# Optimization experiments

Measured on AMD Instinct MI355X. Metric: run time of the kernel, lower is better.

## Reference

```python
import jax, jax.numpy as jnp
import numpy as np

B = 1024
INPUT_DIM = 768
NUM_CLASSES = 5
NUM_PRIMARY_CAPS = 32
PRIMARY_CAP_DIM = 8
ROUTING_CAP_DIM = 16
NUM_ITER = 3
PROJ_DIM = 256 * 6 * 6  # 9216
NUM_IN_CAPS = NUM_PRIMARY_CAPS * 16  # conv output is 4x4 spatial -> 512


def squash(t, axis=-1):
    sq = jnp.sum(t * t, axis=axis, keepdims=True)
    scale = sq / (1.0 + sq)
    return scale * t / jnp.sqrt(sq + 1e-8)


def setup_inputs() -> dict:
    key = jax.random.key(0)
    k = jax.random.split(key, 6)
    x = jax.random.normal(k[0], (B, INPUT_DIM), dtype=jnp.float32)
    W1 = jax.random.normal(k[1], (INPUT_DIM, PROJ_DIM), dtype=jnp.float32) * 0.02
    b1 = jnp.zeros((PROJ_DIM,), dtype=jnp.float32)
    convW = jax.random.normal(k[2], (NUM_PRIMARY_CAPS * PRIMARY_CAP_DIM, 256, 3, 3), dtype=jnp.float32) * 0.02  # OIHW
    convB = jnp.zeros((NUM_PRIMARY_CAPS * PRIMARY_CAP_DIM,), dtype=jnp.float32)
    # matches torch.randn init in RoutingCapsules: [num_in, num_out, out_dim, in_dim]
    Wr = jax.random.normal(k[3], (NUM_IN_CAPS, NUM_CLASSES, ROUTING_CAP_DIM, PRIMARY_CAP_DIM), dtype=jnp.float32)
    return {"x": x, "W1": W1, "b1": b1, "convW": convW, "convB": convB, "Wr": Wr}


def reference(x, W1, b1, convW, convB, Wr):
    # feature projection (dropout is identity in eval)
    h = jax.nn.relu(x @ W1 + b1)
    h = h.reshape(-1, 256, 6, 6)
    # primary capsules conv: k=3, s=1, pad=0 -> [B, 256, 4, 4]
    out = jax.lax.conv_general_dilated(h, convW, window_strides=(1, 1), padding='VALID',
                                       dimension_numbers=('NCHW', 'OIHW', 'NCHW'))
    out = out + convB[None, :, None, None]
    bsz = out.shape[0]
    out = out.reshape(bsz, NUM_PRIMARY_CAPS, PRIMARY_CAP_DIM, -1)      # [B,32,8,16]
    out = jnp.transpose(out, (0, 1, 3, 2)).reshape(bsz, -1, PRIMARY_CAP_DIM)  # [B,512,8]
    u = squash(out, axis=-1)
    # prediction vectors u_hat: [B, in_caps, out_caps, out_dim]
    u_hat = jnp.einsum('nodi,bni->bnod', Wr, u)
    # dynamic routing
    b_logits = jnp.zeros((bsz, NUM_IN_CAPS, NUM_CLASSES, 1), dtype=u_hat.dtype)
    v = None
    for it in range(NUM_ITER):
        c = jax.nn.softmax(b_logits, axis=2)
        s = jnp.sum(c * u_hat, axis=1)  # [B, out_caps, out_dim]
        v = squash(s, axis=-1)
        if it < NUM_ITER - 1:
            agreement = jnp.sum(u_hat * v[:, None], axis=-1, keepdims=True)
            b_logits = b_logits + agreement
    class_probs = jnp.sqrt(jnp.sum(v * v, axis=-1))
    return (class_probs, v)
```

## Files before the change

kernel.cpp:

```cpp
#include <hip/hip_runtime.h>
#include <hip/hip_fp16.h>

#define BSZ   1024
#define INDIM 768
#define PROJ  9216
#define NCAP  512
#define NCLS  5
#define K2    2304

typedef __bf16    bf16x8 __attribute__((ext_vector_type(8)));
typedef _Float16  f16x8  __attribute__((ext_vector_type(8)));
typedef float     f32x4  __attribute__((ext_vector_type(4)));
typedef _Float16  h2     __attribute__((ext_vector_type(2)));

static __device__ __forceinline__ unsigned short f2bf(float f) {
  unsigned int x = __float_as_uint(f);
  return (unsigned short)((x + 0x7fffu + ((x >> 16) & 1u)) >> 16);
}
static __device__ __forceinline__ float bf2f(unsigned int u) {
  return __uint_as_float(u << 16);
}

#if defined(__has_builtin)
#if __has_builtin(__builtin_amdgcn_fdot2)
#define HAVE_FDOT2 1
#endif
#endif
static __device__ __forceinline__ float fdot2(h2 a, h2 b, float c) {
#ifdef HAVE_FDOT2
  return __builtin_amdgcn_fdot2(a, b, c, false);
#else
  return c + (float)a[0] * (float)b[0] + (float)a[1] * (float)b[1];
#endif
}
static __device__ __forceinline__ h2 u2h2(unsigned int u) {
  return __builtin_bit_cast(h2, u);
}
static __device__ __forceinline__ unsigned short f2h(float f) {
  return __builtin_bit_cast(unsigned short, (_Float16)f);
}

static __device__ __forceinline__ void gload16(const void* g, void* l) {
  auto gp = reinterpret_cast<const unsigned int __attribute__((address_space(1)))*>(
      (unsigned long long)g);
  auto lp = reinterpret_cast<unsigned int __attribute__((address_space(3)))*>(
      (unsigned long long)l);
  __builtin_amdgcn_global_load_lds(gp, lp, 16, 0, 0);
}

template <int RELU, int OBF16>
__global__ __launch_bounds__(256) void mfma_gemm(
    const unsigned short* __restrict__ A,
    const unsigned short* __restrict__ Bt,
    const float* __restrict__ bias,
    void* __restrict__ Cout,
    int M, int N, int K) {
  __shared__ __align__(16) unsigned short smem[16384];
  const int t    = threadIdx.x;
  const int bn   = blockIdx.x * 128;
  const int bm   = blockIdx.y * 128;
  const int lane = t & 63;
  const int wid  = t >> 6;
  const int wm   = (wid >> 1) * 64;
  const int wn   = (wid & 1) * 64;
  const int l15  = lane & 15;
  const int kb   = lane >> 4;

  const int r0 = t >> 2,         kc = t & 3;
  const int r1 = (t + 256) >> 2;
  const int gk0 = ((kc ^ (r0 & 3)) << 3);
  const int gk1 = ((kc ^ (r1 & 3)) << 3);

  const unsigned short* Ar0 = A  + (size_t)(bm + r0) * K + gk0;
  const unsigned short* Ar1 = A  + (size_t)(bm + r1) * K + gk1;
  const unsigned short* Br0 = Bt + (size_t)(bn + r0) * K + gk0;
  const unsigned short* Br1 = Bt + (size_t)(bn + r1) * K + gk1;

  int aoff[4], boff[4];
#pragma unroll
  for (int i = 0; i < 4; ++i) {
    const int ra = wm + i * 16 + l15;
    aoff[i] = ra * 32 + ((kb ^ (ra & 3)) << 3);
    const int rb = wn + i * 16 + l15;
    boff[i] = 4096 + rb * 32 + ((kb ^ (rb & 3)) << 3);
  }

  f32x4 acc[4][4];
#pragma unroll
  for (int i = 0; i < 4; ++i)
#pragma unroll
    for (int j = 0; j < 4; ++j)
#pragma unroll
      for (int q = 0; q < 4; ++q) acc[i][j][q] = 0.f;

  const int nk = K >> 5;
  gload16(Ar0, &smem[t * 8]);
  gload16(Ar1, &smem[(t + 256) * 8]);
  gload16(Br0, &smem[4096 + t * 8]);
  gload16(Br1, &smem[4096 + (t + 256) * 8]);
  __syncthreads();

  int buf = 0;
  for (int ks = 0; ks < nk; ++ks) {
    if (ks + 1 < nk) {
      const int k = (ks + 1) << 5;
      const int o = (buf ^ 1) * 8192;
      gload16(Ar0 + k, &smem[o + t * 8]);
      gload16(Ar1 + k, &smem[o + (t + 256) * 8]);
      gload16(Br0 + k, &smem[o + 4096 + t * 8]);
      gload16(Br1 + k, &smem[o + 4096 + (t + 256) * 8]);
    }
    const unsigned short* base = &smem[buf * 8192];
    bf16x8 af[4], bfr[4];
#pragma unroll
    for (int i = 0; i < 4; ++i) {
      af[i]  = *(const bf16x8*)(base + aoff[i]);
      bfr[i] = *(const bf16x8*)(base + boff[i]);
    }
#pragma unroll
    for (int i = 0; i < 4; ++i)
#pragma unroll
      for (int j = 0; j < 4; ++j)
        acc[i][j] = __builtin_amdgcn_mfma_f32_16x16x32_bf16(af[i], bfr[j], acc[i][j], 0, 0, 0);
    __syncthreads();
    buf ^= 1;
  }

#pragma unroll
  for (int j = 0; j < 4; ++j) {
    const int col = bn + wn + j * 16 + l15;
    const float bv = bias[col];
#pragma unroll
    for (int i = 0; i < 4; ++i) {
#pragma unroll
      for (int q = 0; q < 4; ++q) {
        const int row = bm + wm + i * 16 + kb * 4 + q;
        float v = acc[i][j][q] + bv;
        if (RELU) v = fmaxf(v, 0.f);
        if (OBF16) ((unsigned short*)Cout)[(size_t)row * N + col] = f2bf(v);
        else       ((float*)Cout)[(size_t)row * N + col] = v;
      }
    }
  }
}

__global__ __launch_bounds__(256) void conv_gemm_sq(
    const unsigned short* __restrict__ ht,
    const unsigned short* __restrict__ Wt2,
    const float* __restrict__ convB,
    unsigned short* __restrict__ U) {
  __shared__ __align__(16) unsigned short smem[24576];
  const int t    = threadIdx.x;
  const int bn   = blockIdx.x * 128;
  const int bm   = blockIdx.y * 64;
  const int lane = t & 63, wid = t >> 6;
  const int l15  = lane & 15, kb = lane >> 4;

  const unsigned short* asrc[2];
#pragma unroll
  for (int cc = 0; cc < 2; ++cc) {
    const int c = t + cc * 256;
    const int row = c >> 3, seg = c & 7;
    const int gr = bm + row, b = gr >> 4, p = gr & 15;
    const int spb = (p >> 2) * 6 + (p & 3);
    asrc[cc] = ht + (size_t)b * PROJ + spb * 256 + ((seg ^ (row & 7)) << 3);
  }
  const unsigned short* bsrc[4];
#pragma unroll
  for (int cc = 0; cc < 4; ++cc) {
    const int c = t + cc * 256;
    const int row = c >> 3, seg = c & 7;
    bsrc[cc] = Wt2 + (size_t)(bn + row) * K2 + ((seg ^ (row & 7)) << 3);
  }

  int aoff[4][2], boff[2][2];
#pragma unroll
  for (int i = 0; i < 4; ++i)
#pragma unroll
    for (int kk = 0; kk < 2; ++kk) {
      const int row = i * 16 + l15, seg = kk * 4 + kb;
      aoff[i][kk] = row * 64 + ((seg ^ (row & 7)) << 3);
    }
#pragma unroll
  for (int j = 0; j < 2; ++j)
#pragma unroll
    for (int kk = 0; kk < 2; ++kk) {
      const int row = wid * 32 + j * 16 + l15, seg = kk * 4 + kb;
      boff[j][kk] = 4096 + row * 64 + ((seg ^ (row & 7)) << 3);
    }

  f32x4 acc[4][2];
#pragma unroll
  for (int i = 0; i < 4; ++i)
#pragma unroll
    for (int j = 0; j < 2; ++j)
#pragma unroll
      for (int q = 0; q < 4; ++q) acc[i][j][q] = 0.f;

  auto stage = [&](int ks, int buf) {
    const int tap  = ks >> 2;
    const int aofs = (tap + 3 * (tap / 3)) * 256 + ((ks & 3) << 6);
    const int bofs = ks << 6;
    unsigned short* sb = &smem[buf * 12288];
    gload16(asrc[0] + aofs, sb + t * 8);
    gload16(asrc[1] + aofs, sb + t * 8 + 2048);
    gload16(bsrc[0] + bofs, sb + 4096 + t * 8);
    gload16(bsrc[1] + bofs, sb + 4096 + t * 8 + 2048);
    gload16(bsrc[2] + bofs, sb + 4096 + t * 8 + 4096);
    gload16(bsrc[3] + bofs, sb + 4096 + t * 8 + 6144);
  };

  stage(0, 0);
  __syncthreads();

  int buf = 0;
  for (int ks = 0; ks < 36; ++ks) {
    if (ks + 1 < 36) stage(ks + 1, buf ^ 1);
    const unsigned short* base = &smem[buf * 12288];
    bf16x8 af[4][2], bfr[2][2];
#pragma unroll
    for (int i = 0; i < 4; ++i)
#pragma unroll
      for (int kk = 0; kk < 2; ++kk) af[i][kk] = *(const bf16x8*)(base + aoff[i][kk]);
#pragma unroll
    for (int j = 0; j < 2; ++j)
#pragma unroll
      for (int kk = 0; kk < 2; ++kk) bfr[j][kk] = *(const bf16x8*)(base + boff[j][kk]);
#pragma unroll
    for (int kk = 0; kk < 2; ++kk)
#pragma unroll
      for (int i = 0; i < 4; ++i)
#pragma unroll
        for (int j = 0; j < 2; ++j)
          acc[i][j] = __builtin_amdgcn_mfma_f32_16x16x32_bf16(af[i][kk], bfr[j][kk], acc[i][j], 0, 0, 0);
    __syncthreads();
    buf ^= 1;
  }

#pragma unroll
  for (int j = 0; j < 2; ++j) {
    const int oc  = bn + wid * 32 + j * 16 + l15;
    const int cap = oc >> 3, ii = oc & 7;
    const float bv = convB[oc];
#pragma unroll
    for (int i = 0; i < 4; ++i) {
#pragma unroll
      for (int q = 0; q < 4; ++q) {
        const int row = bm + i * 16 + kb * 4 + q;
        const int b = row >> 4, p = row & 15;
        const float val = acc[i][j][q] + bv;
        float sq = val * val;
        sq += __shfl_xor(sq, 1);
        sq += __shfl_xor(sq, 2);
        sq += __shfl_xor(sq, 4);
        const float scale = sq / (1.f + sq) / sqrtf(sq + 1e-8f);
        U[(size_t)b * 4096 + cap * 128 + p * 8 + ii] = f2h(val * scale);
      }
    }
  }
}

__global__ __launch_bounds__(256) void convert_bf16(const float* __restrict__ in,
                                                    unsigned short* __restrict__ out,
                                                    int n4) {
  const int i = blockIdx.x * 256 + threadIdx.x;
  if (i >= n4) return;
  float4 v = ((const float4*)in)[i];
  ushort4 o;
  o.x = f2bf(v.x); o.y = f2bf(v.y); o.z = f2bf(v.z); o.w = f2bf(v.w);
  ((ushort4*)out)[i] = o;
}

__global__ __launch_bounds__(256) void convert_f16(const float* __restrict__ in,
                                                   __half2* __restrict__ out, int n4) {
  const int i = blockIdx.x * 256 + threadIdx.x;
  if (i >= n4) return;
  float4 v = ((const float4*)in)[i];
  out[i * 2]     = __floats2half2_rn(v.x, v.y);
  out[i * 2 + 1] = __floats2half2_rn(v.z, v.w);
}

__global__ __launch_bounds__(256) void transpose_w1_perm(const float* __restrict__ W,
                                                         unsigned short* __restrict__ Wt) {
  __shared__ float tile[32][33];
  const int n0 = blockIdx.x * 32, k0 = blockIdx.y * 32;
  const int r = threadIdx.x >> 3, c = (threadIdx.x & 7) * 4;
  float4 v = *(const float4*)(W + (size_t)(k0 + r) * PROJ + n0 + c);
  tile[r][c] = v.x; tile[r][c + 1] = v.y; tile[r][c + 2] = v.z; tile[r][c + 3] = v.w;
  __syncthreads();
  ushort4 o;
  o.x = f2bf(tile[c + 0][r]); o.y = f2bf(tile[c + 1][r]);
  o.z = f2bf(tile[c + 2][r]); o.w = f2bf(tile[c + 3][r]);
  const int nn = n0 + r;
  const int prow = (nn % 36) * 256 + nn / 36;
  *(ushort4*)(Wt + (size_t)prow * INDIM + k0 + c) = o;
}

__global__ __launch_bounds__(256) void perm_bias(const float* __restrict__ b1,
                                                 float* __restrict__ pb1) {
  const int n = blockIdx.x * 256 + threadIdx.x;
  if (n >= PROJ) return;
  pb1[(n % 36) * 256 + n / 36] = b1[n];
}

__global__ __launch_bounds__(256) void convw_prep2(const float* __restrict__ W,
                                                   unsigned short* __restrict__ Wt2) {
  const int id = blockIdx.x * 256 + threadIdx.x;
  const int oc = id >> 8, ic = id & 255;
  const float* s = W + (size_t)id * 9;
#pragma unroll
  for (int tap = 0; tap < 9; ++tap)
    Wt2[(size_t)oc * K2 + tap * 256 + ic] = f2bf(s[tap]);
}

__global__ __launch_bounds__(512) void uhat_gemm(
    const unsigned short* __restrict__ U,
    const unsigned short* __restrict__ Wrh,
    unsigned short* __restrict__ uhat,
    float* __restrict__ s0q,
    int b0, int CB) {
  __shared__ float sred[8][16][80];
  const int mt = blockIdx.x, q = blockIdx.y;
  const int t = threadIdx.x, wid = t >> 6, lane = t & 63;
  const int l15 = lane & 15, kb = lane >> 4;
  const int bm = mt * 16;
  const int gb = b0 + bm;

  f32x4 sacc[5];
#pragma unroll
  for (int j = 0; j < 5; ++j)
#pragma unroll
    for (int r = 0; r < 4; ++r) sacc[j][r] = 0.f;

  const uint4 zz = make_uint4(0, 0, 0, 0);
#pragma unroll
  for (int i = 0; i < 8; ++i) {
    const int n = q * 64 + wid * 8 + i;
    uint4 av = zz;
    if (kb == 0) av = *(const uint4*)(U + (size_t)(gb + l15) * 4096 + n * 8);
    const f16x8 uf = __builtin_bit_cast(f16x8, av);
#pragma unroll
    for (int jn = 0; jn < 5; ++jn) {
      uint4 wv = zz;
      if (kb == 0) wv = *(const uint4*)(Wrh + (size_t)n * 640 + (jn * 16 + l15) * 8);
      f32x4 z;
      z[0] = 0.f; z[1] = 0.f; z[2] = 0.f; z[3] = 0.f;
      f32x4 c = __builtin_amdgcn_mfma_f32_16x16x32_f16(
          __builtin_bit_cast(f16x8, wv), uf, z, 0, 0, 0);
      ushort4 st;
      st.x = f2h(c[0]); st.y = f2h(c[1]); st.z = f2h(c[2]); st.w = f2h(c[3]);
      *(ushort4*)(uhat + ((size_t)(bm + l15) * 512 + n) * 80 + jn * 16 + kb * 4) = st;
#pragma unroll
      for (int qq = 0; qq < 4; ++qq) sacc[jn][qq] += c[qq];
    }
  }

#pragma unroll
  for (int jn = 0; jn < 5; ++jn)
#pragma unroll
    for (int qq = 0; qq < 4; ++qq)
      sred[wid][l15][jn * 16 + kb * 4 + qq] = sacc[jn][qq];
  __syncthreads();
#pragma unroll
  for (int k = 0; k < 3; ++k) {
    const int id = t + k * 512;
    if (id < 1280) {
      const int bb = id / 80, od = id % 80;
      float val = 0.f;
#pragma unroll
      for (int w = 0; w < 8; ++w) val += sred[w][bb][od];
      s0q[((size_t)q * CB + bm + bb) * 80 + od] = val;
    }
  }
}

template <int MODE>
__global__ __launch_bounds__(256) void route_pass(
    const unsigned short* __restrict__ uhat,
    const float* __restrict__ s0q,
    const float* __restrict__ vsum_in,
    float* __restrict__ vsum_out,
    float* __restrict__ out,
    int b0, int CB) {
  __shared__ unsigned int vph2[40];
  __shared__ float red[4][2][40];
  const int bl = blockIdx.x;
  const int b  = b0 + bl;
  const int t  = threadIdx.x;

  float v0r = 0.f;
  if (t < 80) {
    if (MODE == 1) {
      float s = 0.f;
#pragma unroll
      for (int g = 0; g < 8; ++g) s += s0q[((size_t)g * CB + bl) * 80 + t];
      s *= 0.2f;
      float sq = s * s;
      sq += __shfl_xor(sq, 1);
      sq += __shfl_xor(sq, 2);
      sq += __shfl_xor(sq, 4);
      sq += __shfl_xor(sq, 8);
      const float scale = sq / (1.f + sq) / sqrtf(sq + 1e-8f);
      v0r = s * scale;
    } else {
      v0r = vsum_in[(size_t)bl * 80 + t];
    }
    const float vnext = __shfl_down(v0r, 1);
    if ((t & 1) == 0)
      vph2[t >> 1] = __builtin_bit_cast(unsigned int, __floats2half2_rn(v0r, vnext));
  }
  __syncthreads();

  const int p = t >> 1, h = t & 1;
  float acc[5][8];
#pragma unroll
  for (int o = 0; o < 5; ++o)
#pragma unroll
    for (int j = 0; j < 8; ++j) acc[o][j] = 0.f;

  const unsigned short* ub = uhat + (size_t)bl * 40960;
  for (int c4 = 0; c4 < 4; ++c4) {
    const int n = c4 * 128 + p;
    const unsigned short* row = ub + n * 80 + h * 8;
    uint4 uv[5];
#pragma unroll
    for (int o = 0; o < 5; ++o) uv[o] = *(const uint4*)(row + o * 16);
    float ap[5];
#pragma unroll
    for (int o = 0; o < 5; ++o) {
      const int vb = o * 8 + h * 4;
      float a = fdot2(u2h2(uv[o].x), u2h2(vph2[vb]), 0.f);
      a = fdot2(u2h2(uv[o].y), u2h2(vph2[vb + 1]), a);
      a = fdot2(u2h2(uv[o].z), u2h2(vph2[vb + 2]), a);
      a = fdot2(u2h2(uv[o].w), u2h2(vph2[vb + 3]), a);
      ap[o] = a + __shfl_xor(a, 1);
    }
    float m = ap[0];
#pragma unroll
    for (int o = 1; o < 5; ++o) m = fmaxf(m, ap[o]);
    float es = 0.f, e[5];
#pragma unroll
    for (int o = 0; o < 5; ++o) { e[o] = __expf(ap[o] - m); es += e[o]; }
    const float inv = 1.f / es;
#pragma unroll
    for (int o = 0; o < 5; ++o) {
      const float cc = e[o] * inv;
      h2 hx = u2h2(uv[o].x), hy = u2h2(uv[o].y), hz = u2h2(uv[o].z), hw = u2h2(uv[o].w);
      acc[o][0] += cc * (float)hx[0]; acc[o][1] += cc * (float)hx[1];
      acc[o][2] += cc * (float)hy[0]; acc[o][3] += cc * (float)hy[1];
      acc[o][4] += cc * (float)hz[0]; acc[o][5] += cc * (float)hz[1];
      acc[o][6] += cc * (float)hw[0]; acc[o][7] += cc * (float)hw[1];
    }
  }

#pragma unroll
  for (int off = 2; off <= 32; off <<= 1)
#pragma unroll
    for (int o = 0; o < 5; ++o)
#pragma unroll
      for (int j = 0; j < 8; ++j) acc[o][j] += __shfl_xor(acc[o][j], off);
  const int wid = t >> 6, lane = t & 63;
  if (lane < 2) {
#pragma unroll
    for (int o = 0; o < 5; ++o)
#pragma unroll
      for (int j = 0; j < 8; ++j) red[wid][lane][o * 8 + j] = acc[o][j];
  }
  __syncthreads();

  if (t < 80) {
    const int o = t >> 4, d = t & 15, hh = d >> 3, dl = d & 7;
    const int c = o * 8 + dl;
    float s = red[0][hh][c] + red[1][hh][c] + red[2][hh][c] + red[3][hh][c];
    float sq = s * s;
    sq += __shfl_xor(sq, 1);
    sq += __shfl_xor(sq, 2);
    sq += __shfl_xor(sq, 4);
    sq += __shfl_xor(sq, 8);
    const float scale = sq / (1.f + sq) / sqrtf(sq + 1e-8f);
    const float vn = s * scale;
    if (MODE == 1) {
      vsum_out[(size_t)bl * 80 + t] = v0r + vn;
    } else {
      out[5 * BSZ + (size_t)b * 80 + t] = vn;
      float vv = vn * vn;
      vv += __shfl_xor(vv, 1);
      vv += __shfl_xor(vv, 2);
      vv += __shfl_xor(vv, 4);
      vv += __shfl_xor(vv, 8);
      if ((t & 15) == 0) out[(size_t)b * 5 + o] = sqrtf(vv);
    }
  }
}

extern "C" void kernel_launch(void* const* d_in, const int* in_sizes, int n_in,
                              void* d_out, int out_size, void* d_ws, size_t ws_size,
                              hipStream_t stream) {
  const float* x     = (const float*)d_in[0];
  const float* W1    = (const float*)d_in[1];
  const float* b1    = (const float*)d_in[2];
  const float* convW = (const float*)d_in[3];
  const float* convB = (const float*)d_in[4];
  const float* Wr    = (const float*)d_in[5];
  float* out = (float*)d_out;

  char* base = (char*)d_ws;
  size_t off = 0;
  auto alloc = [&](size_t bytes) { size_t o = off; off = (off + bytes + 255) & ~(size_t)255; return o; };
  const size_t o_wrh  = alloc((size_t)NCAP * 640 * 2);
  const size_t o_u    = alloc((size_t)BSZ * 4096 * 2);
  const size_t o_s0q  = alloc((size_t)8 * BSZ * 80 * 4);
  const size_t o_vsum = alloc((size_t)BSZ * 80 * 4);
  const size_t o_pool = off;
  size_t poff = o_pool;
  auto palloc = [&](size_t bytes) { size_t o = poff; poff = (poff + bytes + 255) & ~(size_t)255; return o; };
  const size_t o_ht  = palloc((size_t)BSZ * PROJ * 2);
  const size_t o_w1t = palloc((size_t)PROJ * INDIM * 2);
  const size_t o_xb  = palloc((size_t)BSZ * INDIM * 2);
  const size_t o_wt2 = palloc((size_t)256 * K2 * 2);
  const size_t o_pb1 = palloc((size_t)PROJ * 4);

  unsigned short* ht   = (unsigned short*)(base + o_ht);
  unsigned short* w1t  = (unsigned short*)(base + o_w1t);
  unsigned short* xb   = (unsigned short*)(base + o_xb);
  unsigned short* wt2  = (unsigned short*)(base + o_wt2);
  float*          pb1  = (float*)(base + o_pb1);
  unsigned short* wrh  = (unsigned short*)(base + o_wrh);
  unsigned short* u    = (unsigned short*)(base + o_u);
  float*          s0q  = (float*)(base + o_s0q);
  float*          vsum = (float*)(base + o_vsum);
  unsigned short* uhat = (unsigned short*)(base + o_pool);

  convert_bf16<<<(BSZ * INDIM / 4 + 255) / 256, 256, 0, stream>>>(x, xb, BSZ * INDIM / 4);
  transpose_w1_perm<<<dim3(PROJ / 32, INDIM / 32), 256, 0, stream>>>(W1, w1t);
  perm_bias<<<PROJ / 256, 256, 0, stream>>>(b1, pb1);
  convw_prep2<<<256, 256, 0, stream>>>(convW, wt2);
  convert_f16<<<(NCAP * 640 / 4 + 255) / 256, 256, 0, stream>>>(Wr, (__half2*)wrh, NCAP * 640 / 4);

  mfma_gemm<1, 1><<<dim3(PROJ / 128, BSZ / 128), 256, 0, stream>>>(
      xb, w1t, pb1, (void*)ht, BSZ, PROJ, INDIM);

  conv_gemm_sq<<<dim3(2, 256), 256, 0, stream>>>(ht, wt2, convB, u);

  const size_t pool_sz = ws_size > o_pool ? ws_size - o_pool : 0;
  int CB = 1024;
  while (CB > 16 && (size_t)CB * 512 * 80 * 2 > pool_sz) CB >>= 1;
  for (int b0 = 0; b0 < BSZ; b0 += CB) {
    uhat_gemm<<<dim3(CB / 16, 8), 512, 0, stream>>>(
        u, wrh, uhat, s0q, b0, CB);
    route_pass<1><<<CB, 256, 0, stream>>>(uhat, s0q, nullptr, vsum, out, b0, CB);
    route_pass<2><<<CB, 256, 0, stream>>>(uhat, nullptr, vsum, nullptr, out, b0, CB);
  }
}
```

Baseline: 152.8 us.

## Recompute u_hat per routing pass instead of materializing it in memory

Replaces the stored fp16 u_hat tensor with on-the-fly MFMA recomputation inside three fused routing kernels. Each pass rebuilds the previous v from per-group partial sums, computes agreement and softmax in registers, and writes new partial sums. This removes the large u_hat write and two rereads in exchange for redundant small GEMMs. The small preprocessing kernels are also merged into a single launch.

Result: slower. 157.0 us (+2.7%).

```diff
diff --git a/kernel.cpp b/kernel.cpp
--- a/kernel.cpp
+++ b/kernel.cpp
@@ -19,22 +19,6 @@
 }
 static __device__ __forceinline__ float bf2f(unsigned int u) {
   return __uint_as_float(u << 16);
-}
-
-#if defined(__has_builtin)
-#if __has_builtin(__builtin_amdgcn_fdot2)
-#define HAVE_FDOT2 1
-#endif
-#endif
-static __device__ __forceinline__ float fdot2(h2 a, h2 b, float c) {
-#ifdef HAVE_FDOT2
-  return __builtin_amdgcn_fdot2(a, b, c, false);
-#else
-  return c + (float)a[0] * (float)b[0] + (float)a[1] * (float)b[1];
-#endif
-}
-static __device__ __forceinline__ h2 u2h2(unsigned int u) {
-  return __builtin_bit_cast(h2, u);
 }
 static __device__ __forceinline__ unsigned short f2h(float f) {
   return __builtin_bit_cast(unsigned short, (_Float16)f);
@@ -260,24 +244,39 @@
   }
 }
 
-__global__ __launch_bounds__(256) void convert_bf16(const float* __restrict__ in,
-                                                    unsigned short* __restrict__ out,
-                                                    int n4) {
-  const int i = blockIdx.x * 256 + threadIdx.x;
-  if (i >= n4) return;
-  float4 v = ((const float4*)in)[i];
-  ushort4 o;
-  o.x = f2bf(v.x); o.y = f2bf(v.y); o.z = f2bf(v.z); o.w = f2bf(v.w);
-  ((ushort4*)out)[i] = o;
-}
-
-__global__ __launch_bounds__(256) void convert_f16(const float* __restrict__ in,
-                                                   __half2* __restrict__ out, int n4) {
-  const int i = blockIdx.x * 256 + threadIdx.x;
-  if (i >= n4) return;
-  float4 v = ((const float4*)in)[i];
-  out[i * 2]     = __floats2half2_rn(v.x, v.y);
-  out[i * 2 + 1] = __floats2half2_rn(v.z, v.w);
+#define NX_ITEMS (BSZ * INDIM / 4)
+#define NW_ITEMS (NCAP * 640 / 4)
+#define NC_ITEMS 65536
+#define NB_ITEMS PROJ
+#define PREP_TOTAL (NX_ITEMS + NW_ITEMS + NC_ITEMS + NB_ITEMS)
+
+__global__ __launch_bounds__(256) void prep_small(
+    const float* __restrict__ x, unsigned short* __restrict__ xb,
+    const float* __restrict__ Wr, __half2* __restrict__ wrh,
+    const float* __restrict__ convW, unsigned short* __restrict__ wt2,
+    const float* __restrict__ b1, float* __restrict__ pb1) {
+  const int id = blockIdx.x * 256 + threadIdx.x;
+  if (id < NX_ITEMS) {
+    float4 v = ((const float4*)x)[id];
+    ushort4 o;
+    o.x = f2bf(v.x); o.y = f2bf(v.y); o.z = f2bf(v.z); o.w = f2bf(v.w);
+    ((ushort4*)xb)[id] = o;
+  } else if (id < NX_ITEMS + NW_ITEMS) {
+    const int i = id - NX_ITEMS;
+    float4 v = ((const float4*)Wr)[i];
+    wrh[i * 2]     = __floats2half2_rn(v.x, v.y);
+    wrh[i * 2 + 1] = __floats2half2_rn(v.z, v.w);
+  } else if (id < NX_ITEMS + NW_ITEMS + NC_ITEMS) {
+    const int i = id - NX_ITEMS - NW_ITEMS;
+    const int oc = i >> 8, ic = i & 255;
+    const float* s = convW + (size_t)i * 9;
+#pragma unroll
+    for (int tap = 0; tap < 9; ++tap)
+      wt2[(size_t)oc * K2 + tap * 256 + ic] = f2bf(s[tap]);
+  } else if (id < PREP_TOTAL) {
+    const int n = id - NX_ITEMS - NW_ITEMS - NC_ITEMS;
+    pb1[(n % 36) * 256 + n / 36] = b1[n];
+  }
 }
 
 __global__ __launch_bounds__(256) void transpose_w1_perm(const float* __restrict__ W,
@@ -296,41 +295,68 @@
   *(ushort4*)(Wt + (size_t)prow * INDIM + k0 + c) = o;
 }
 
-__global__ __launch_bounds__(256) void perm_bias(const float* __restrict__ b1,
-                                                 float* __restrict__ pb1) {
-  const int n = blockIdx.x * 256 + threadIdx.x;
-  if (n >= PROJ) return;
-  pb1[(n % 36) * 256 + n / 36] = b1[n];
-}
-
-__global__ __launch_bounds__(256) void convw_prep2(const float* __restrict__ W,
-                                                   unsigned short* __restrict__ Wt2) {
-  const int id = blockIdx.x * 256 + threadIdx.x;
-  const int oc = id >> 8, ic = id & 255;
-  const float* s = W + (size_t)id * 9;
-#pragma unroll
-  for (int tap = 0; tap < 9; ++tap)
-    Wt2[(size_t)oc * K2 + tap * 256 + ic] = f2bf(s[tap]);
-}
-
-__global__ __launch_bounds__(512) void uhat_gemm(
+template <int MODE>
+__global__ __launch_bounds__(512) void route_fused(
     const unsigned short* __restrict__ U,
     const unsigned short* __restrict__ Wrh,
-    unsigned short* __restrict__ uhat,
-    float* __restrict__ s0q,
-    int b0, int CB) {
+    const float* __restrict__ sp0,
+    const float* __restrict__ sp1,
+    float* __restrict__ spout) {
   __shared__ float sred[8][16][80];
+  __shared__ float s0l[16][81];
+  __shared__ float s1l[16][81];
+  __shared__ float scl[16][5][2];
   const int mt = blockIdx.x, q = blockIdx.y;
   const int t = threadIdx.x, wid = t >> 6, lane = t & 63;
   const int l15 = lane & 15, kb = lane >> 4;
-  const int bm = mt * 16;
-  const int gb = b0 + bm;
+  const int gb = mt * 16;
+
+  float vreg[5][4];
+  if (MODE >= 1) {
+    for (int item = t; item < 1280; item += 512) {
+      const int bl = item / 80, od = item % 80;
+      float a0 = 0.f, a1 = 0.f;
+#pragma unroll
+      for (int g = 0; g < 8; ++g) {
+        a0 += sp0[((size_t)g * BSZ + gb + bl) * 80 + od];
+        if (MODE == 2) a1 += sp1[((size_t)g * BSZ + gb + bl) * 80 + od];
+      }
+      s0l[bl][od] = a0 * 0.2f;
+      if (MODE == 2) s1l[bl][od] = a1;
+    }
+    __syncthreads();
+    if (t < 80) {
+      const int bl = t / 5, o = t % 5;
+      float sq0 = 0.f, sq1 = 0.f;
+#pragma unroll
+      for (int d = 0; d < 16; ++d) {
+        const float x0 = s0l[bl][o * 16 + d];
+        sq0 += x0 * x0;
+        if (MODE == 2) { const float x1 = s1l[bl][o * 16 + d]; sq1 += x1 * x1; }
+      }
+      scl[bl][o][0] = sq0 / (1.f + sq0) / sqrtf(sq0 + 1e-8f);
+      if (MODE == 2) scl[bl][o][1] = sq1 / (1.f + sq1) / sqrtf(sq1 + 1e-8f);
+    }
+    __syncthreads();
+#pragma unroll
+    for (int jn = 0; jn < 5; ++jn) {
+      const float sc0 = scl[l15][jn][0];
+      const float sc1 = (MODE == 2) ? scl[l15][jn][1] : 0.f;
+#pragma unroll
+      for (int qq = 0; qq < 4; ++qq) {
+        const int od = jn * 16 + kb * 4 + qq;
+        float v = s0l[l15][od] * sc0;
+        if (MODE == 2) v += s1l[l15][od] * sc1;
+        vreg[jn][qq] = v;
+      }
+    }
+  }
 
   f32x4 sacc[5];
 #pragma unroll
-  for (int j = 0; j < 5; ++j)
-#pragma unroll
-    for (int r = 0; r < 4; ++r) sacc[j][r] = 0.f;
+  for (int jn = 0; jn < 5; ++jn)
+#pragma unroll
+    for (int qq = 0; qq < 4; ++qq) sacc[jn][qq] = 0.f;
 
   const uint4 zz = make_uint4(0, 0, 0, 0);
 #pragma unroll
@@ -339,20 +365,42 @@
     uint4 av = zz;
     if (kb == 0) av = *(const uint4*)(U + (size_t)(gb + l15) * 4096 + n * 8);
     const f16x8 uf = __builtin_bit_cast(f16x8, av);
+    f32x4 cfr[5];
 #pragma unroll
     for (int jn = 0; jn < 5; ++jn) {
       uint4 wv = zz;
       if (kb == 0) wv = *(const uint4*)(Wrh + (size_t)n * 640 + (jn * 16 + l15) * 8);
       f32x4 z;
       z[0] = 0.f; z[1] = 0.f; z[2] = 0.f; z[3] = 0.f;
-      f32x4 c = __builtin_amdgcn_mfma_f32_16x16x32_f16(
+      cfr[jn] = __builtin_amdgcn_mfma_f32_16x16x32_f16(
           __builtin_bit_cast(f16x8, wv), uf, z, 0, 0, 0);
-      ushort4 st;
-      st.x = f2h(c[0]); st.y = f2h(c[1]); st.z = f2h(c[2]); st.w = f2h(c[3]);
-      *(ushort4*)(uhat + ((size_t)(bm + l15) * 512 + n) * 80 + jn * 16 + kb * 4) = st;
-#pragma unroll
-      for (int qq = 0; qq < 4; ++qq) sacc[jn][qq] += c[qq];
-    }
+    }
+    float c[5];
+    if (MODE == 0) {
+#pragma unroll
+      for (int o = 0; o < 5; ++o) c[o] = 1.f;
+    } else {
+      float a[5];
+#pragma unroll
+      for (int jn = 0; jn < 5; ++jn) {
+        float d = cfr[jn][0] * vreg[jn][0] + cfr[jn][1] * vreg[jn][1] +
+                  cfr[jn][2] * vreg[jn][2] + cfr[jn][3] * vreg[jn][3];
+        d += __shfl_xor(d, 16);
+        d += __shfl_xor(d, 32);
+        a[jn] = d;
+      }
+      float m = fmaxf(fmaxf(fmaxf(a[0], a[1]), fmaxf(a[2], a[3])), a[4]);
+      float es = 0.f;
+#pragma unroll
+      for (int o = 0; o < 5; ++o) { c[o] = __expf(a[o] - m); es += c[o]; }
+      const float inv = 1.f / es;
+#pragma unroll
+      for (int o = 0; o < 5; ++o) c[o] *= inv;
+    }
+#pragma unroll
+    for (int jn = 0; jn < 5; ++jn)
+#pragma unroll
+      for (int qq = 0; qq < 4; ++qq) sacc[jn][qq] += c[jn] * cfr[jn][qq];
   }
 
 #pragma unroll
@@ -369,109 +417,18 @@
       float val = 0.f;
 #pragma unroll
       for (int w = 0; w < 8; ++w) val += sred[w][bb][od];
-      s0q[((size_t)q * CB + bm + bb) * 80 + od] = val;
-    }
-  }
-}
-
-template <int MODE>
-__global__ __launch_bounds__(256) void route_pass(
-    const unsigned short* __restrict__ uhat,
-    const float* __restrict__ s0q,
-    const float* __restrict__ vsum_in,
-    float* __restrict__ vsum_out,
-    float* __restrict__ out,
-    int b0, int CB) {
-  __shared__ unsigned int vph2[40];
-  __shared__ float red[4][2][40];
-  const int bl = blockIdx.x;
-  const int b  = b0 + bl;
-  const int t  = threadIdx.x;
-
-  float v0r = 0.f;
+      spout[((size_t)q * BSZ + gb + bb) * 80 + od] = val;
+    }
+  }
+}
+
+__global__ __launch_bounds__(128) void route_emit(
+    const float* __restrict__ sp2, float* __restrict__ out) {
+  const int b = blockIdx.x, t = threadIdx.x;
   if (t < 80) {
-    if (MODE == 1) {
-      float s = 0.f;
-#pragma unroll
-      for (int g = 0; g < 8; ++g) s += s0q[((size_t)g * CB + bl) * 80 + t];
-      s *= 0.2f;
-      float sq = s * s;
-      sq += __shfl_xor(sq, 1);
-      sq += __shfl_xor(sq, 2);
-      sq += __shfl_xor(sq, 4);
-      sq += __shfl_xor(sq, 8);
-      const float scale = sq / (1.f + sq) / sqrtf(sq + 1e-8f);
-      v0r = s * scale;
-    } else {
-      v0r = vsum_in[(size_t)bl * 80 + t];
-    }
-    const float vnext = __shfl_down(v0r, 1);
-    if ((t & 1) == 0)
-      vph2[t >> 1] = __builtin_bit_cast(unsigned int, __floats2half2_rn(v0r, vnext));
-  }
-  __syncthreads();
-
-  const int p = t >> 1, h = t & 1;
-  float acc[5][8];
-#pragma unroll
-  for (int o = 0; o < 5; ++o)
-#pragma unroll
-    for (int j = 0; j < 8; ++j) acc[o][j] = 0.f;
-
-  const unsigned short* ub = uhat + (size_t)bl * 40960;
-  for (int c4 = 0; c4 < 4; ++c4) {
-    const int n = c4 * 128 + p;
-    const unsigned short* row = ub + n * 80 + h * 8;
-    uint4 uv[5];
-#pragma unroll
-    for (int o = 0; o < 5; ++o) uv[o] = *(const uint4*)(row + o * 16);
-    float ap[5];
-#pragma unroll
-    for (int o = 0; o < 5; ++o) {
-      const int vb = o * 8 + h * 4;
-      float a = fdot2(u2h2(uv[o].x), u2h2(vph2[vb]), 0.f);
-      a = fdot2(u2h2(uv[o].y), u2h2(vph2[vb + 1]), a);
-      a = fdot2(u2h2(uv[o].z), u2h2(vph2[vb + 2]), a);
-      a = fdot2(u2h2(uv[o].w), u2h2(vph2[vb + 3]), a);
-      ap[o] = a + __shfl_xor(a, 1);
-    }
-    float m = ap[0];
-#pragma unroll
-    for (int o = 1; o < 5; ++o) m = fmaxf(m, ap[o]);
-    float es = 0.f, e[5];
-#pragma unroll
-    for (int o = 0; o < 5; ++o) { e[o] = __expf(ap[o] - m); es += e[o]; }
-    const float inv = 1.f / es;
-#pragma unroll
-    for (int o = 0; o < 5; ++o) {
-      const float cc = e[o] * inv;
-      h2 hx = u2h2(uv[o].x), hy = u2h2(uv[o].y), hz = u2h2(uv[o].z), hw = u2h2(uv[o].w);
-      acc[o][0] += cc * (float)hx[0]; acc[o][1] += cc * (float)hx[1];
-      acc[o][2] += cc * (float)hy[0]; acc[o][3] += cc * (float)hy[1];
-      acc[o][4] += cc * (float)hz[0]; acc[o][5] += cc * (float)hz[1];
-      acc[o][6] += cc * (float)hw[0]; acc[o][7] += cc * (float)hw[1];
-    }
-  }
-
-#pragma unroll
-  for (int off = 2; off <= 32; off <<= 1)
-#pragma unroll
-    for (int o = 0; o < 5; ++o)
-#pragma unroll
-      for (int j = 0; j < 8; ++j) acc[o][j] += __shfl_xor(acc[o][j], off);
-  const int wid = t >> 6, lane = t & 63;
-  if (lane < 2) {
-#pragma unroll
-    for (int o = 0; o < 5; ++o)
-#pragma unroll
-      for (int j = 0; j < 8; ++j) red[wid][lane][o * 8 + j] = acc[o][j];
-  }
-  __syncthreads();
-
-  if (t < 80) {
-    const int o = t >> 4, d = t & 15, hh = d >> 3, dl = d & 7;
-    const int c = o * 8 + dl;
-    float s = red[0][hh][c] + red[1][hh][c] + red[2][hh][c] + red[3][hh][c];
+    float s = 0.f;
+#pragma unroll
+    for (int g = 0; g < 8; ++g) s += sp2[((size_t)g * BSZ + b) * 80 + t];
     float sq = s * s;
     sq += __shfl_xor(sq, 1);
     sq += __shfl_xor(sq, 2);
@@ -479,17 +436,13 @@
     sq += __shfl_xor(sq, 8);
     const float scale = sq / (1.f + sq) / sqrtf(sq + 1e-8f);
     const float vn = s * scale;
-    if (MODE == 1) {
-      vsum_out[(size_t)bl * 80 + t] = v0r + vn;
-    } else {
-      out[5 * BSZ + (size_t)b * 80 + t] = vn;
-      float vv = vn * vn;
-      vv += __shfl_xor(vv, 1);
-      vv += __shfl_xor(vv, 2);
-      vv += __shfl_xor(vv, 4);
-      vv += __shfl_xor(vv, 8);
-      if ((t & 15) == 0) out[(size_t)b * 5 + o] = sqrtf(vv);
-    }
+    out[5 * BSZ + (size_t)b * 80 + t] = vn;
+    float vv = vn * vn;
+    vv += __shfl_xor(vv, 1);
+    vv += __shfl_xor(vv, 2);
+    vv += __shfl_xor(vv, 4);
+    vv += __shfl_xor(vv, 8);
+    if ((t & 15) == 0) out[(size_t)b * 5 + (t >> 4)] = sqrtf(vv);
   }
 }
 
@@ -507,48 +460,40 @@
   char* base = (char*)d_ws;
   size_t off = 0;
   auto alloc = [&](size_t bytes) { size_t o = off; off = (off + bytes + 255) & ~(size_t)255; return o; };
-  const size_t o_wrh  = alloc((size_t)NCAP * 640 * 2);
-  const size_t o_u    = alloc((size_t)BSZ * 4096 * 2);
-  const size_t o_s0q  = alloc((size_t)8 * BSZ * 80 * 4);
-  const size_t o_vsum = alloc((size_t)BSZ * 80 * 4);
-  const size_t o_pool = off;
-  size_t poff = o_pool;
-  auto palloc = [&](size_t bytes) { size_t o = poff; poff = (poff + bytes + 255) & ~(size_t)255; return o; };
-  const size_t o_ht  = palloc((size_t)BSZ * PROJ * 2);
-  const size_t o_w1t = palloc((size_t)PROJ * INDIM * 2);
-  const size_t o_xb  = palloc((size_t)BSZ * INDIM * 2);
-  const size_t o_wt2 = palloc((size_t)256 * K2 * 2);
-  const size_t o_pb1 = palloc((size_t)PROJ * 4);
-
-  unsigned short* ht   = (unsigned short*)(base + o_ht);
-  unsigned short* w1t  = (unsigned short*)(base + o_w1t);
-  unsigned short* xb   = (unsigned short*)(base + o_xb);
-  unsigned short* wt2  = (unsigned short*)(base + o_wt2);
-  float*          pb1  = (float*)(base + o_pb1);
-  unsigned short* wrh  = (unsigned short*)(base + o_wrh);
-  unsigned short* u    = (unsigned short*)(base + o_u);
-  float*          s0q  = (float*)(base + o_s0q);
-  float*          vsum = (float*)(base + o_vsum);
-  unsigned short* uhat = (unsigned short*)(base + o_pool);
-
-  convert_bf16<<<(BSZ * INDIM / 4 + 255) / 256, 256, 0, stream>>>(x, xb, BSZ * INDIM / 4);
+  const size_t o_wrh = alloc((size_t)NCAP * 640 * 2);
+  const size_t o_u   = alloc((size_t)BSZ * 4096 * 2);
+  const size_t o_sp0 = alloc((size_t)8 * BSZ * 80 * 4);
+  const size_t o_sp1 = alloc((size_t)8 * BSZ * 80 * 4);
+  const size_t o_sp2 = alloc((size_t)8 * BSZ * 80 * 4);
+  const size_t o_ht  = alloc((size_t)BSZ * PROJ * 2);
+  const size_t o_w1t = alloc((size_t)PROJ * INDIM * 2);
+  const size_t o_xb  = alloc((size_t)BSZ * INDIM * 2);
+  const size_t o_wt2 = alloc((size_t)256 * K2 * 2);
+  const size_t o_pb1 = alloc((size_t)PROJ * 4);
+
+  unsigned short* wrh = (unsigned short*)(base + o_wrh);
+  unsigned short* u   = (unsigned short*)(base + o_u);
+  float*          sp0 = (float*)(base + o_sp0);
+  float*          sp1 = (float*)(base + o_sp1);
+  float*          sp2 = (float*)(base + o_sp2);
+  unsigned short* ht  = (unsigned short*)(base + o_ht);
+  unsigned short* w1t = (unsigned short*)(base + o_w1t);
+  unsigned short* xb  = (unsigned short*)(base + o_xb);
+  unsigned short* wt2 = (unsigned short*)(base + o_wt2);
+  float*          pb1 = (float*)(base + o_pb1);
+
+  prep_small<<<(PREP_TOTAL + 255) / 256, 256, 0, stream>>>(
+      x, xb, Wr, (__half2*)wrh, convW, wt2, b1, pb1);
   transpose_w1_perm<<<dim3(PROJ / 32, INDIM / 32), 256, 0, stream>>>(W1, w1t);
-  perm_bias<<<PROJ / 256, 256, 0, stream>>>(b1, pb1);
-  convw_prep2<<<256, 256, 0, stream>>>(convW, wt2);
-  convert_f16<<<(NCAP * 640 / 4 + 255) / 256, 256, 0, stream>>>(Wr, (__half2*)wrh, NCAP * 640 / 4);
 
   mfma_gemm<1, 1><<<dim3(PROJ / 128, BSZ / 128), 256, 0, stream>>>(
       xb, w1t, pb1, (void*)ht, BSZ, PROJ, INDIM);
 
   conv_gemm_sq<<<dim3(2, 256), 256, 0, stream>>>(ht, wt2, convB, u);
 
-  const size_t pool_sz = ws_size > o_pool ? ws_size - o_pool : 0;
-  int CB = 1024;
-  while (CB > 16 && (size_t)CB * 512 * 80 * 2 > pool_sz) CB >>= 1;
-  for (int b0 = 0; b0 < BSZ; b0 += CB) {
-    uhat_gemm<<<dim3(CB / 16, 8), 512, 0, stream>>>(
-        u, wrh, uhat, s0q, b0, CB);
-    route_pass<1><<<CB, 256, 0, stream>>>(uhat, s0q, nullptr, vsum, out, b0, CB);
-    route_pass<2><<<CB, 256, 0, stream>>>(uhat, nullptr, vsum, nullptr, out, b0, CB);
-  }
-}
+  dim3 fg(BSZ / 16, 8);
+  route_fused<0><<<fg, 512, 0, stream>>>(u, wrh, nullptr, nullptr, sp0);
+  route_fused<1><<<fg, 512, 0, stream>>>(u, wrh, sp0, nullptr, sp1);
+  route_fused<2><<<fg, 512, 0, stream>>>(u, wrh, sp0, sp1, sp2);
+  route_emit<<<BSZ, 128, 0, stream>>>(sp2, out);
+}
```

## Deepen GEMM K-tile to 64, enlarge conv tile to 128x128, fuse prep kernels

Applied to the files above, without the earlier changes.

The projection GEMM now stages 64-wide K slices with an XOR swizzle over 8 segments, which halves the number of loop iterations and barriers. The conv GEMM moves from a 64x128 to a 128x128 block tile with a 2x2 wave layout, giving more reuse per LDS load. Four small preprocessing kernels are merged into one launch to cut launch overhead. In exchange, each block uses more LDS (64KB) and more accumulator registers, which may lower occupancy, and the conv grid is halved.

Result: slower. 157.0 us (+2.8%).

```diff
diff --git a/kernel.cpp b/kernel.cpp
--- a/kernel.cpp
+++ b/kernel.cpp
@@ -19,6 +19,9 @@
 }
 static __device__ __forceinline__ float bf2f(unsigned int u) {
   return __uint_as_float(u << 16);
+}
+static __device__ __forceinline__ unsigned short f2h(float f) {
+  return __builtin_bit_cast(unsigned short, (_Float16)f);
 }
 
 #if defined(__has_builtin)
@@ -36,9 +39,6 @@
 static __device__ __forceinline__ h2 u2h2(unsigned int u) {
   return __builtin_bit_cast(h2, u);
 }
-static __device__ __forceinline__ unsigned short f2h(float f) {
-  return __builtin_bit_cast(unsigned short, (_Float16)f);
-}
 
 static __device__ __forceinline__ void gload16(const void* g, void* l) {
   auto gp = reinterpret_cast<const unsigned int __attribute__((address_space(1)))*>(
@@ -48,42 +48,42 @@
   __builtin_amdgcn_global_load_lds(gp, lp, 16, 0, 0);
 }
 
-template <int RELU, int OBF16>
-__global__ __launch_bounds__(256) void mfma_gemm(
+__global__ __launch_bounds__(256) void mfma_gemm_bk64(
     const unsigned short* __restrict__ A,
     const unsigned short* __restrict__ Bt,
     const float* __restrict__ bias,
-    void* __restrict__ Cout,
+    unsigned short* __restrict__ Cout,
     int M, int N, int K) {
-  __shared__ __align__(16) unsigned short smem[16384];
+  __shared__ __align__(16) unsigned short smem[32768];
   const int t    = threadIdx.x;
   const int bn   = blockIdx.x * 128;
   const int bm   = blockIdx.y * 128;
-  const int lane = t & 63;
-  const int wid  = t >> 6;
+  const int lane = t & 63, wid = t >> 6;
   const int wm   = (wid >> 1) * 64;
   const int wn   = (wid & 1) * 64;
-  const int l15  = lane & 15;
-  const int kb   = lane >> 4;
-
-  const int r0 = t >> 2,         kc = t & 3;
-  const int r1 = (t + 256) >> 2;
-  const int gk0 = ((kc ^ (r0 & 3)) << 3);
-  const int gk1 = ((kc ^ (r1 & 3)) << 3);
-
-  const unsigned short* Ar0 = A  + (size_t)(bm + r0) * K + gk0;
-  const unsigned short* Ar1 = A  + (size_t)(bm + r1) * K + gk1;
-  const unsigned short* Br0 = Bt + (size_t)(bn + r0) * K + gk0;
-  const unsigned short* Br1 = Bt + (size_t)(bn + r1) * K + gk1;
-
-  int aoff[4], boff[4];
-#pragma unroll
-  for (int i = 0; i < 4; ++i) {
-    const int ra = wm + i * 16 + l15;
-    aoff[i] = ra * 32 + ((kb ^ (ra & 3)) << 3);
-    const int rb = wn + i * 16 + l15;
-    boff[i] = 4096 + rb * 32 + ((kb ^ (rb & 3)) << 3);
-  }
+  const int l15  = lane & 15, kb = lane >> 4;
+
+  const unsigned short* asrc[4];
+  const unsigned short* bsrc[4];
+#pragma unroll
+  for (int cc = 0; cc < 4; ++cc) {
+    const int c = t + cc * 256;
+    const int row = c >> 3, seg = c & 7;
+    const int sk = (seg ^ (row & 7)) << 3;
+    asrc[cc] = A  + (size_t)(bm + row) * K + sk;
+    bsrc[cc] = Bt + (size_t)(bn + row) * K + sk;
+  }
+
+  int aoff[4][2], boff[4][2];
+#pragma unroll
+  for (int i = 0; i < 4; ++i)
+#pragma unroll
+    for (int kk = 0; kk < 2; ++kk) {
+      const int ra = wm + i * 16 + l15, sa = kk * 4 + kb;
+      aoff[i][kk] = ra * 64 + ((sa ^ (ra & 7)) << 3);
+      const int rb = wn + i * 16 + l15;
+      boff[i][kk] = 8192 + rb * 64 + ((sa ^ (rb & 7)) << 3);
+    }
 
   f32x4 acc[4][4];
 #pragma unroll
@@ -93,35 +93,39 @@
 #pragma unroll
       for (int q = 0; q < 4; ++q) acc[i][j][q] = 0.f;
 
-  const int nk = K >> 5;
-  gload16(Ar0, &smem[t * 8]);
-  gload16(Ar1, &smem[(t + 256) * 8]);
-  gload16(Br0, &smem[4096 + t * 8]);
-  gload16(Br1, &smem[4096 + (t + 256) * 8]);
+  const int nk = K >> 6;
+  auto stage = [&](int ks, int buf) {
+    const int ko = ks << 6;
+    unsigned short* sb = &smem[buf * 16384];
+#pragma unroll
+    for (int cc = 0; cc < 4; ++cc) {
+      gload16(asrc[cc] + ko, sb + (t + cc * 256) * 8);
+      gload16(bsrc[cc] + ko, sb + 8192 + (t + cc * 256) * 8);
+    }
+  };
+
+  stage(0, 0);
   __syncthreads();
 
   int buf = 0;
   for (int ks = 0; ks < nk; ++ks) {
-    if (ks + 1 < nk) {
-      const int k = (ks + 1) << 5;
-      const int o = (buf ^ 1) * 8192;
-      gload16(Ar0 + k, &smem[o + t * 8]);
-      gload16(Ar1 + k, &smem[o + (t + 256) * 8]);
-      gload16(Br0 + k, &smem[o + 4096 + t * 8]);
-      gload16(Br1 + k, &smem[o + 4096 + (t + 256) * 8]);
-    }
-    const unsigned short* base = &smem[buf * 8192];
-    bf16x8 af[4], bfr[4];
-#pragma unroll
-    for (int i = 0; i < 4; ++i) {
-      af[i]  = *(const bf16x8*)(base + aoff[i]);
-      bfr[i] = *(const bf16x8*)(base + boff[i]);
-    }
+    if (ks + 1 < nk) stage(ks + 1, buf ^ 1);
+    const unsigned short* base = &smem[buf * 16384];
+    bf16x8 af[4][2], bfr[4][2];
 #pragma unroll
     for (int i = 0; i < 4; ++i)
 #pragma unroll
-      for (int j = 0; j < 4; ++j)
-        acc[i][j] = __builtin_amdgcn_mfma_f32_16x16x32_bf16(af[i], bfr[j], acc[i][j], 0, 0, 0);
+      for (int kk = 0; kk < 2; ++kk) {
+        af[i][kk]  = *(const bf16x8*)(base + aoff[i][kk]);
+        bfr[i][kk] = *(const bf16x8*)(base + boff[i][kk]);
+      }
+#pragma unroll
+    for (int kk = 0; kk < 2; ++kk)
+#pragma unroll
+      for (int i = 0; i < 4; ++i)
+#pragma unroll
+        for (int j = 0; j < 4; ++j)
+          acc[i][j] = __builtin_amdgcn_mfma_f32_16x16x32_bf16(af[i][kk], bfr[j][kk], acc[i][j], 0, 0, 0);
     __syncthreads();
     buf ^= 1;
   }
@@ -131,69 +135,57 @@
     const int col = bn + wn + j * 16 + l15;
     const float bv = bias[col];
 #pragma unroll
-    for (int i = 0; i < 4; ++i) {
+    for (int i = 0; i < 4; ++i)
 #pragma unroll
       for (int q = 0; q < 4; ++q) {
         const int row = bm + wm + i * 16 + kb * 4 + q;
-        float v = acc[i][j][q] + bv;
-        if (RELU) v = fmaxf(v, 0.f);
-        if (OBF16) ((unsigned short*)Cout)[(size_t)row * N + col] = f2bf(v);
-        else       ((float*)Cout)[(size_t)row * N + col] = v;
+        Cout[(size_t)row * N + col] = f2bf(fmaxf(acc[i][j][q] + bv, 0.f));
       }
-    }
-  }
-}
-
-__global__ __launch_bounds__(256) void conv_gemm_sq(
+  }
+}
+
+__global__ __launch_bounds__(256) void conv_gemm_sq128(
     const unsigned short* __restrict__ ht,
     const unsigned short* __restrict__ Wt2,
     const float* __restrict__ convB,
     unsigned short* __restrict__ U) {
-  __shared__ __align__(16) unsigned short smem[24576];
+  __shared__ __align__(16) unsigned short smem[32768];
   const int t    = threadIdx.x;
   const int bn   = blockIdx.x * 128;
-  const int bm   = blockIdx.y * 64;
+  const int bm   = blockIdx.y * 128;
   const int lane = t & 63, wid = t >> 6;
+  const int wm   = (wid >> 1) * 64;
+  const int wn   = (wid & 1) * 64;
   const int l15  = lane & 15, kb = lane >> 4;
 
-  const unsigned short* asrc[2];
-#pragma unroll
-  for (int cc = 0; cc < 2; ++cc) {
+  const unsigned short* asrc[4];
+  const unsigned short* bsrc[4];
+#pragma unroll
+  for (int cc = 0; cc < 4; ++cc) {
     const int c = t + cc * 256;
     const int row = c >> 3, seg = c & 7;
     const int gr = bm + row, b = gr >> 4, p = gr & 15;
     const int spb = (p >> 2) * 6 + (p & 3);
     asrc[cc] = ht + (size_t)b * PROJ + spb * 256 + ((seg ^ (row & 7)) << 3);
-  }
-  const unsigned short* bsrc[4];
-#pragma unroll
-  for (int cc = 0; cc < 4; ++cc) {
-    const int c = t + cc * 256;
-    const int row = c >> 3, seg = c & 7;
     bsrc[cc] = Wt2 + (size_t)(bn + row) * K2 + ((seg ^ (row & 7)) << 3);
   }
 
-  int aoff[4][2], boff[2][2];
+  int aoff[4][2], boff[4][2];
 #pragma unroll
   for (int i = 0; i < 4; ++i)
 #pragma unroll
     for (int kk = 0; kk < 2; ++kk) {
-      const int row = i * 16 + l15, seg = kk * 4 + kb;
-      aoff[i][kk] = row * 64 + ((seg ^ (row & 7)) << 3);
-    }
-#pragma unroll
-  for (int j = 0; j < 2; ++j)
-#pragma unroll
-    for (int kk = 0; kk < 2; ++kk) {
-      const int row = wid * 32 + j * 16 + l15, seg = kk * 4 + kb;
-      boff[j][kk] = 4096 + row * 64 + ((seg ^ (row & 7)) << 3);
-    }
-
-  f32x4 acc[4][2];
+      const int ra = wm + i * 16 + l15, sa = kk * 4 + kb;
+      aoff[i][kk] = ra * 64 + ((sa ^ (ra & 7)) << 3);
+      const int rb = wn + i * 16 + l15;
+      boff[i][kk] = 8192 + rb * 64 + ((sa ^ (rb & 7)) << 3);
+    }
+
+  f32x4 acc[4][4];
 #pragma unroll
   for (int i = 0; i < 4; ++i)
 #pragma unroll
-    for (int j = 0; j < 2; ++j)
+    for (int j = 0; j < 4; ++j)
 #pragma unroll
       for (int q = 0; q < 4; ++q) acc[i][j][q] = 0.f;
 
@@ -201,13 +193,12 @@
     const int tap  = ks >> 2;
     const int aofs = (tap + 3 * (tap / 3)) * 256 + ((ks & 3) << 6);
     const int bofs = ks << 6;
-    unsigned short* sb = &smem[buf * 12288];
-    gload16(asrc[0] + aofs, sb + t * 8);
-    gload16(asrc[1] + aofs, sb + t * 8 + 2048);
-    gload16(bsrc[0] + bofs, sb + 4096 + t * 8);
-    gload16(bsrc[1] + bofs, sb + 4096 + t * 8 + 2048);
-    gload16(bsrc[2] + bofs, sb + 4096 + t * 8 + 4096);
-    gload16(bsrc[3] + bofs, sb + 4096 + t * 8 + 6144);
+    unsigned short* sb = &smem[buf * 16384];
+#pragma unroll
+    for (int cc = 0; cc < 4; ++cc) {
+      gload16(asrc[cc] + aofs, sb + (t + cc * 256) * 8);
+      gload16(bsrc[cc] + bofs, sb + 8192 + (t + cc * 256) * 8);
+    }
   };
 
   stage(0, 0);
@@ -216,37 +207,36 @@
   int buf = 0;
   for (int ks = 0; ks < 36; ++ks) {
     if (ks + 1 < 36) stage(ks + 1, buf ^ 1);
-    const unsigned short* base = &smem[buf * 12288];
-    bf16x8 af[4][2], bfr[2][2];
+    const unsigned short* base = &smem[buf * 16384];
+    bf16x8 af[4][2], bfr[4][2];
 #pragma unroll
     for (int i = 0; i < 4; ++i)
 #pragma unroll
-      for (int kk = 0; kk < 2; ++kk) af[i][kk] = *(const bf16x8*)(base + aoff[i][kk]);
-#pragma unroll
-    for (int j = 0; j < 2; ++j)
-#pragma unroll
-      for (int kk = 0; kk < 2; ++kk) bfr[j][kk] = *(const bf16x8*)(base + boff[j][kk]);
+      for (int kk = 0; kk < 2; ++kk) {
+        af[i][kk]  = *(const bf16x8*)(base + aoff[i][kk]);
+        bfr[i][kk] = *(const bf16x8*)(base + boff[i][kk]);
+      }
 #pragma unroll
     for (int kk = 0; kk < 2; ++kk)
 #pragma unroll
       for (int i = 0; i < 4; ++i)
 #pragma unroll
-        for (int j = 0; j < 2; ++j)
+        for (int j = 0; j < 4; ++j)
           acc[i][j] = __builtin_amdgcn_mfma_f32_16x16x32_bf16(af[i][kk], bfr[j][kk], acc[i][j], 0, 0, 0);
     __syncthreads();
     buf ^= 1;
   }
 
 #pragma unroll
-  for (int j = 0; j < 2; ++j) {
-    const int oc  = bn + wid * 32 + j * 16 + l15;
+  for (int j = 0; j < 4; ++j) {
+    const int oc  = bn + wn + j * 16 + l15;
     const int cap = oc >> 3, ii = oc & 7;
     const float bv = convB[oc];
 #pragma unroll
-    for (int i = 0; i < 4; ++i) {
+    for (int i = 0; i < 4; ++i)
 #pragma unroll
       for (int q = 0; q < 4; ++q) {
-        const int row = bm + i * 16 + kb * 4 + q;
+        const int row = bm + wm + i * 16 + kb * 4 + q;
         const int b = row >> 4, p = row & 15;
         const float val = acc[i][j][q] + bv;
         float sq = val * val;
@@ -256,28 +246,42 @@
         const float scale = sq / (1.f + sq) / sqrtf(sq + 1e-8f);
         U[(size_t)b * 4096 + cap * 128 + p * 8 + ii] = f2h(val * scale);
       }
-    }
-  }
-}
-
-__global__ __launch_bounds__(256) void convert_bf16(const float* __restrict__ in,
-                                                    unsigned short* __restrict__ out,
-                                                    int n4) {
-  const int i = blockIdx.x * 256 + threadIdx.x;
-  if (i >= n4) return;
-  float4 v = ((const float4*)in)[i];
-  ushort4 o;
-  o.x = f2bf(v.x); o.y = f2bf(v.y); o.z = f2bf(v.z); o.w = f2bf(v.w);
-  ((ushort4*)out)[i] = o;
-}
-
-__global__ __launch_bounds__(256) void convert_f16(const float* __restrict__ in,
-                                                   __half2* __restrict__ out, int n4) {
-  const int i = blockIdx.x * 256 + threadIdx.x;
-  if (i >= n4) return;
-  float4 v = ((const float4*)in)[i];
-  out[i * 2]     = __floats2half2_rn(v.x, v.y);
-  out[i * 2 + 1] = __floats2half2_rn(v.z, v.w);
+  }
+}
+
+#define NX_ITEMS (BSZ * INDIM / 4)
+#define NW_ITEMS (NCAP * 640 / 4)
+#define NC_ITEMS 65536
+#define NB_ITEMS PROJ
+#define PREP_TOTAL (NX_ITEMS + NW_ITEMS + NC_ITEMS + NB_ITEMS)
+
+__global__ __launch_bounds__(256) void prep_small(
+    const float* __restrict__ x, unsigned short* __restrict__ xb,
+    const float* __restrict__ Wr, __half2* __restrict__ wrh,
+    const float* __restrict__ convW, unsigned short* __restrict__ wt2,
+    const float* __restrict__ b1, float* __restrict__ pb1) {
+  const int id = blockIdx.x * 256 + threadIdx.x;
+  if (id < NX_ITEMS) {
+    float4 v = ((const float4*)x)[id];
+    ushort4 o;
+    o.x = f2bf(v.x); o.y = f2bf(v.y); o.z = f2bf(v.z); o.w = f2bf(v.w);
+    ((ushort4*)xb)[id] = o;
+  } else if (id < NX_ITEMS + NW_ITEMS) {
+    const int i = id - NX_ITEMS;
+    float4 v = ((const float4*)Wr)[i];
+    wrh[i * 2]     = __floats2half2_rn(v.x, v.y);
+    wrh[i * 2 + 1] = __floats2half2_rn(v.z, v.w);
+  } else if (id < NX_ITEMS + NW_ITEMS + NC_ITEMS) {
+    const int i = id - NX_ITEMS - NW_ITEMS;
+    const int oc = i >> 8, ic = i & 255;
+    const float* s = convW + (size_t)i * 9;
+#pragma unroll
+    for (int tap = 0; tap < 9; ++tap)
+      wt2[(size_t)oc * K2 + tap * 256 + ic] = f2bf(s[tap]);
+  } else if (id < PREP_TOTAL) {
+    const int n = id - NX_ITEMS - NW_ITEMS - NC_ITEMS;
+    pb1[(n % 36) * 256 + n / 36] = b1[n];
+  }
 }
 
 __global__ __launch_bounds__(256) void transpose_w1_perm(const float* __restrict__ W,
@@ -294,23 +298,6 @@
   const int nn = n0 + r;
   const int prow = (nn % 36) * 256 + nn / 36;
   *(ushort4*)(Wt + (size_t)prow * INDIM + k0 + c) = o;
-}
-
-__global__ __launch_bounds__(256) void perm_bias(const float* __restrict__ b1,
-                                                 float* __restrict__ pb1) {
-  const int n = blockIdx.x * 256 + threadIdx.x;
-  if (n >= PROJ) return;
-  pb1[(n % 36) * 256 + n / 36] = b1[n];
-}
-
-__global__ __launch_bounds__(256) void convw_prep2(const float* __restrict__ W,
-                                                   unsigned short* __restrict__ Wt2) {
-  const int id = blockIdx.x * 256 + threadIdx.x;
-  const int oc = id >> 8, ic = id & 255;
-  const float* s = W + (size_t)id * 9;
-#pragma unroll
-  for (int tap = 0; tap < 9; ++tap)
-    Wt2[(size_t)oc * K2 + tap * 256 + ic] = f2bf(s[tap]);
 }
 
 __global__ __launch_bounds__(512) void uhat_gemm(
@@ -531,23 +518,20 @@
   float*          vsum = (float*)(base + o_vsum);
   unsigned short* uhat = (unsigned short*)(base + o_pool);
 
-  convert_bf16<<<(BSZ * INDIM / 4 + 255) / 256, 256, 0, stream>>>(x, xb, BSZ * INDIM / 4);
+  prep_small<<<(PREP_TOTAL + 255) / 256, 256, 0, stream>>>(
+      x, xb, Wr, (__half2*)wrh, convW, wt2, b1, pb1);
   transpose_w1_perm<<<dim3(PROJ / 32, INDIM / 32), 256, 0, stream>>>(W1, w1t);
-  perm_bias<<<PROJ / 256, 256, 0, stream>>>(b1, pb1);
-  convw_prep2<<<256, 256, 0, stream>>>(convW, wt2);
-  convert_f16<<<(NCAP * 640 / 4 + 255) / 256, 256, 0, stream>>>(Wr, (__half2*)wrh, NCAP * 640 / 4);
-
-  mfma_gemm<1, 1><<<dim3(PROJ / 128, BSZ / 128), 256, 0, stream>>>(
-      xb, w1t, pb1, (void*)ht, BSZ, PROJ, INDIM);
-
-  conv_gemm_sq<<<dim3(2, 256), 256, 0, stream>>>(ht, wt2, convB, u);
+
+  mfma_gemm_bk64<<<dim3(PROJ / 128, BSZ / 128), 256, 0, stream>>>(
+      xb, w1t, pb1, ht, BSZ, PROJ, INDIM);
+
+  conv_gemm_sq128<<<dim3(2, 128), 256, 0, stream>>>(ht, wt2, convB, u);
 
   const size_t pool_sz = ws_size > o_pool ? ws_size - o_pool : 0;
   int CB = 1024;
   while (CB > 16 && (size_t)CB * 512 * 80 * 2 > pool_sz) CB >>= 1;
   for (int b0 = 0; b0 < BSZ; b0 += CB) {
-    uhat_gemm<<<dim3(CB / 16, 8), 512, 0, stream>>>(
-        u, wrh, uhat, s0q, b0, CB);
+    uhat_gemm<<<dim3(CB / 16, 8), 512, 0, stream>>>(u, wrh, uhat, s0q, b0, CB);
     route_pass<1><<<CB, 256, 0, stream>>>(uhat, s0q, nullptr, vsum, out, b0, CB);
     route_pass<2><<<CB, 256, 0, stream>>>(uhat, nullptr, vsum, nullptr, out, b0, CB);
   }
```
